# Kernel tuning notes

Measured on AMD Instinct MI355X. Metric: run time of the kernel, lower is better.

Reference implementation:

```python
import jax, jax.numpy as jnp
import numpy as np

E = 16          # num_experts
H = 2048        # hidden_size
I = 768         # moe_intermediate_size
T = 2048        # tokens (batch*seq)
K = 2           # top_k


def setup_inputs() -> dict:
    key = jax.random.key(0)
    k1, k2, k3, k4, k5 = jax.random.split(key, 5)
    hidden_states = jax.random.normal(k1, (T, H), dtype=jnp.float32)
    top_k_index = jax.random.randint(k2, (T, K), 0, E, dtype=jnp.int32)
    w = jax.random.uniform(k3, (T, K), dtype=jnp.float32)
    top_k_weights = w / jnp.sum(w, axis=-1, keepdims=True)  # softmax-like router weights
    init_std = 0.02
    gate_up_proj = jax.random.normal(k4, (E, 2 * I, H), dtype=jnp.float32) * init_std
    down_proj = jax.random.normal(k5, (E, H, I), dtype=jnp.float32) * init_std
    return {
        "hidden_states": hidden_states,
        "top_k_index": top_k_index,
        "top_k_weights": top_k_weights,
        "gate_up_proj": gate_up_proj,
        "down_proj": down_proj,
    }


def reference(hidden_states, top_k_index, top_k_weights, gate_up_proj, down_proj):
    # Combine matrix C[t, e] = sum_k top_k_weights[t, k] * 1[top_k_index[t,k] == e]
    # Tokens not routed to expert e get weight 0, so the dense-masked compute
    # below is mathematically identical to the per-expert gather/scatter loop.
    t_idx = jnp.arange(T)[:, None]
    C = jnp.zeros((T, E), dtype=hidden_states.dtype).at[t_idx, top_k_index].add(top_k_weights)

    # gate/up projection for every (token, expert): [T, E, 2I]
    gu = jnp.einsum('th,egh->teg', hidden_states, gate_up_proj)
    gate, up = jnp.split(gu, 2, axis=-1)                  # [T, E, I] each
    mid = jax.nn.silu(gate) * up                          # SwiGLU, [T, E, I]
    # down projection fused with routed combine weights -> [T, H]
    out = jnp.einsum('tei,ehi,te->th', mid, down_proj, C)
    return out
```

## Files before the change

kernel.cpp:

```cpp
#include <hip/hip_runtime.h>

#define TTOK  2048
#define HID   2048
#define IMID  768
#define NEXP  16
#define NPAIR 4096
#define NSLOT 4224
#define BM    128
#define BK    64
#define MAXT  48
#define LDB   72
#define ABUF  (128 * 64)

typedef __attribute__((ext_vector_type(8))) short  short8;
typedef __attribute__((ext_vector_type(4))) float  floatx4;
typedef __attribute__((ext_vector_type(2))) unsigned uint2v;

__device__ __forceinline__ unsigned pk2(float a, float b) {
    union { float f; unsigned u; } x{a}, y{b};
    unsigned ra = (x.u + 0x7FFFu + ((x.u >> 16) & 1u)) >> 16;
    unsigned rb = (y.u + 0x7FFFu + ((y.u >> 16) & 1u)) & 0xFFFF0000u;
    return ra | rb;
}

__device__ __forceinline__ short f2bf(float f) {
    union { float f; unsigned u; } v; v.f = f;
    return (short)((v.u + 0x7FFFu + ((v.u >> 16) & 1u)) >> 16);
}

__device__ __forceinline__ short8 cvt8(float4 a, float4 b) {
    union { unsigned u[4]; short8 s; } r;
    r.u[0] = pk2(a.x, a.y); r.u[1] = pk2(a.z, a.w);
    r.u[2] = pk2(b.x, b.y); r.u[3] = pk2(b.z, b.w);
    return r.s;
}

__device__ __forceinline__ void async_cp16(const void* g, void* l) {
    __builtin_amdgcn_global_load_lds(
        (const __attribute__((address_space(1))) void*)g,
        (__attribute__((address_space(3))) void*)l, 16, 0, 0);
}

__global__ __launch_bounds__(256) void k_pre(
    const float* __restrict__ hs, const int* __restrict__ idx,
    const float* __restrict__ tkw, int* __restrict__ ntiles,
    int4* __restrict__ tiles, int* __restrict__ tok,
    float* __restrict__ wgt, short* __restrict__ X)
{
    const int tid = threadIdx.x;
    if (blockIdx.x == 0) {
        __shared__ int cnt[NEXP], cur[NEXP];
        if (tid < NEXP) cnt[tid] = 0;
        __syncthreads();
        for (int i = tid; i < NPAIR; i += 256) atomicAdd(&cnt[idx[i]], 1);
        __syncthreads();
        if (tid == 0) {
            int s = 0, nt = 0;
            for (int e = 0; e < NEXP; e++) {
                cur[e] = s;
                int n = cnt[e];
                for (int tt = 0; tt * BM < n; tt++) {
                    tiles[nt] = make_int4(e, s + tt * BM, min(BM, n - tt * BM), 0);
                    nt++;
                }
                s += n;
            }
            *ntiles = nt;
        }
        __syncthreads();
        for (int i = tid; i < NPAIR; i += 256) {
            int e = idx[i];
            int p = atomicAdd(&cur[e], 1);
            tok[p] = i >> 1;
            wgt[p] = tkw[i];
        }
        for (int i = NPAIR + tid; i < NSLOT; i += 256) { tok[i] = 0; wgt[i] = 0.0f; }
    } else {
        const int row = blockIdx.x - 1;
        const float* src = hs + (size_t)row * HID + tid * 8;
        float4 a = *(const float4*)src;
        float4 b = *(const float4*)(src + 4);
        *(short8*)(X + (size_t)row * HID + tid * 8) = cvt8(a, b);
    }
}

__global__ __launch_bounds__(256, 2) void k_gemm1(
    const float* __restrict__ gup, const short* __restrict__ X,
    const int* __restrict__ ntiles, const int4* __restrict__ tiles,
    const int* __restrict__ tok, const float* __restrict__ wgt,
    short* __restrict__ mid)
{
    if ((int)blockIdx.y >= *ntiles) return;
    const int4 td = tiles[blockIdx.y];
    const int e = td.x, rowstart = td.y, nvalid = td.z;
    const int ct = blockIdx.x;

    __shared__ short sA[2 * ABUF];
    __shared__ short sB[128 * LDB];
    __shared__ int   s_tok[BM];
    __shared__ float s_w[BM];

    const int tid = threadIdx.x;
    if (tid < BM) { s_tok[tid] = tok[rowstart + tid]; s_w[tid] = wgt[rowstart + tid]; }
    __syncthreads();

    const int wave = tid >> 6, lane = tid & 63;
    const int m16 = lane & 15, quad = lane >> 4;

    const int lrow = tid >> 3;
    const int gsw  = (tid & 7) ^ (lrow & 7);
    const short* aga[4];
#pragma unroll
    for (int j = 0; j < 4; j++)
        aga[j] = X + (size_t)s_tok[lrow + j * 32] * HID + gsw * 8;

    const int colgrp = tid & 15;
    const int rowoff = tid >> 4;
    const float* bgate = gup + ((size_t)e * (2 * IMID) + ct * 64) * HID;
    const float* bup   = bgate + (size_t)IMID * HID;

    float4 br[8];
    auto loadB = [&](int k0) {
#pragma unroll
        for (int i = 0; i < 8; i++) {
            int brow = i * 16 + rowoff;
            const float* p = (i < 4) ? (bgate + (size_t)brow * HID)
                                     : (bup + (size_t)(brow - 64) * HID);
            br[i] = *(const float4*)(p + k0 + colgrp * 4);
        }
    };
    auto issueA = [&](int k0, short* dst) {
#pragma unroll
        for (int j = 0; j < 4; j++)
            async_cp16(aga[j] + k0, dst + j * 2048 + wave * 512);
    };

    const int Wm = (wave >> 1) << 6;
    const int Wi = (wave & 1) << 5;
    floatx4 ag[4][2], au[4][2];
#pragma unroll
    for (int a = 0; a < 4; a++)
#pragma unroll
        for (int b = 0; b < 2; b++) { ag[a][b] = (floatx4)0.0f; au[a][b] = (floatx4)0.0f; }

    loadB(0);
    issueA(0, sA);

    const int nsteps = HID / BK;
    for (int ks = 0; ks < nsteps; ks++) {
        short* Acur  = sA + (ks & 1) * ABUF;
        short* Anext = sA + ((ks + 1) & 1) * ABUF;

#pragma unroll
        for (int i = 0; i < 8; i++) {
            int brow = i * 16 + rowoff;
            uint2v w2;
            w2.x = pk2(br[i].x, br[i].y);
            w2.y = pk2(br[i].z, br[i].w);
            *(uint2v*)&sB[brow * LDB + colgrp * 4] = w2;
        }
        __syncthreads();

        if (ks + 1 < nsteps) {
            issueA((ks + 1) * BK, Anext);
            loadB((ks + 1) * BK);
        }

#pragma unroll
        for (int h = 0; h < 2; h++) {
            short8 af[4];
#pragma unroll
            for (int mf = 0; mf < 4; mf++) {
                int row = Wm + mf * 16 + m16;
                int gc = (h * 4 + quad) ^ (row & 7);
                af[mf] = *(const short8*)&Acur[row * 64 + gc * 8];
            }
#pragma unroll
            for (int nf = 0; nf < 2; nf++) {
                const short8 bg = *(const short8*)&sB[(Wi + nf * 16 + m16) * LDB + h * 32 + quad * 8];
                const short8 bu = *(const short8*)&sB[(64 + Wi + nf * 16 + m16) * LDB + h * 32 + quad * 8];
#pragma unroll
                for (int mf = 0; mf < 4; mf++) {
                    ag[mf][nf] = __builtin_amdgcn_mfma_f32_16x16x32_bf16(af[mf], bg, ag[mf][nf], 0, 0, 0);
                    au[mf][nf] = __builtin_amdgcn_mfma_f32_16x16x32_bf16(af[mf], bu, au[mf][nf], 0, 0, 0);
                }
            }
        }
        __syncthreads();
    }

#pragma unroll
    for (int mf = 0; mf < 4; mf++) {
#pragma unroll
        for (int r = 0; r < 4; r++) {
            int m = Wm + mf * 16 + quad * 4 + r;
            if (m < nvalid) {
                float w = s_w[m];
                size_t rowp = (size_t)(rowstart + m) * IMID + ct * 64;
#pragma unroll
                for (int nf = 0; nf < 2; nf++) {
                    float g = ag[mf][nf][r], u = au[mf][nf][r];
                    float val = g / (1.0f + __expf(-g)) * u * w;
                    mid[rowp + Wi + nf * 16 + m16] = f2bf(val);
                }
            }
        }
    }
}

__global__ __launch_bounds__(256, 2) void k_gemm2(
    const float* __restrict__ down, const short* __restrict__ mid,
    const int* __restrict__ ntiles, const int4* __restrict__ tiles,
    const int* __restrict__ tok, float* __restrict__ out)
{
    if ((int)blockIdx.y >= *ntiles) return;
    const int4 td = tiles[blockIdx.y];
    const int e = td.x, rowstart = td.y, nvalid = td.z;
    const int ct = blockIdx.x;

    __shared__ short sA[2 * ABUF];
    __shared__ short sB[128 * LDB];
    __shared__ int   s_tok[BM];

    const int tid = threadIdx.x;
    if (tid < BM) s_tok[tid] = tok[rowstart + tid];
    __syncthreads();

    const int wave = tid >> 6, lane = tid & 63;
    const int m16 = lane & 15, quad = lane >> 4;

    const int lrow = tid >> 3;
    const int gsw  = (tid & 7) ^ (lrow & 7);
    const short* aga[4];
#pragma unroll
    for (int j = 0; j < 4; j++)
        aga[j] = mid + (size_t)(rowstart + lrow + j * 32) * IMID + gsw * 8;

    const int colgrp = tid & 15;
    const int rowoff = tid >> 4;
    const float* bbase = down + ((size_t)e * HID + ct * 128) * IMID;

    float4 br[8];
    auto loadB = [&](int k0) {
#pragma unroll
        for (int i = 0; i < 8; i++)
            br[i] = *(const float4*)(bbase + (size_t)(i * 16 + rowoff) * IMID + k0 + colgrp * 4);
    };
    auto issueA = [&](int k0, short* dst) {
#pragma unroll
        for (int j = 0; j < 4; j++)
            async_cp16(aga[j] + k0, dst + j * 2048 + wave * 512);
    };

    const int Wm = (wave >> 1) << 6;
    const int Wn = (wave & 1) << 6;
    floatx4 acc[4][4];
#pragma unroll
    for (int a = 0; a < 4; a++)
#pragma unroll
        for (int b = 0; b < 4; b++) acc[a][b] = (floatx4)0.0f;

    loadB(0);
    issueA(0, sA);

    const int nsteps = IMID / BK;
    for (int ks = 0; ks < nsteps; ks++) {
        short* Acur  = sA + (ks & 1) * ABUF;
        short* Anext = sA + ((ks + 1) & 1) * ABUF;

#pragma unroll
        for (int i = 0; i < 8; i++) {
            int brow = i * 16 + rowoff;
            uint2v w2;
            w2.x = pk2(br[i].x, br[i].y);
            w2.y = pk2(br[i].z, br[i].w);
            *(uint2v*)&sB[brow * LDB + colgrp * 4] = w2;
        }
        __syncthreads();

        if (ks + 1 < nsteps) {
            issueA((ks + 1) * BK, Anext);
            loadB((ks + 1) * BK);
        }

#pragma unroll
        for (int h = 0; h < 2; h++) {
            short8 af[4];
#pragma unroll
            for (int mf = 0; mf < 4; mf++) {
                int row = Wm + mf * 16 + m16;
                int gc = (h * 4 + quad) ^ (row & 7);
                af[mf] = *(const short8*)&Acur[row * 64 + gc * 8];
            }
#pragma unroll
            for (int nf = 0; nf < 4; nf++) {
                const short8 bf_ = *(const short8*)&sB[(Wn + nf * 16 + m16) * LDB + h * 32 + quad * 8];
#pragma unroll
                for (int mf = 0; mf < 4; mf++)
                    acc[mf][nf] = __builtin_amdgcn_mfma_f32_16x16x32_bf16(af[mf], bf_, acc[mf][nf], 0, 0, 0);
            }
        }
        __syncthreads();
    }

#pragma unroll
    for (int mf = 0; mf < 4; mf++) {
#pragma unroll
        for (int r = 0; r < 4; r++) {
            int m = Wm + mf * 16 + quad * 4 + r;
            if (m < nvalid) {
                int t = s_tok[m];
                float* op = out + (size_t)t * HID + ct * 128;
#pragma unroll
                for (int nf = 0; nf < 4; nf++)
                    atomicAdd(op + Wn + nf * 16 + m16, acc[mf][nf][r]);
            }
        }
    }
}

extern "C" void kernel_launch(void* const* d_in, const int* in_sizes, int n_in,
                              void* d_out, int out_size, void* d_ws, size_t ws_size,
                              hipStream_t stream) {
    const float* hs   = (const float*)d_in[0];
    const int*   idx  = (const int*)d_in[1];
    const float* tkw  = (const float*)d_in[2];
    const float* gup  = (const float*)d_in[3];
    const float* down = (const float*)d_in[4];
    float* out = (float*)d_out;

    char* ws = (char*)d_ws;
    int*   ntiles = (int*)ws;
    int4*  tiles  = (int4*)(ws + 16);
    int*   tok    = (int*)(ws + 1024);
    float* wgt    = (float*)(ws + 1024 + NSLOT * 4);
    short* mid    = (short*)(ws + 36864);
    short* X      = (short*)(ws + 36864 + (size_t)NSLOT * IMID * 2);

    hipMemsetAsync(d_out, 0, (size_t)TTOK * HID * sizeof(float), stream);
    k_pre  <<<2049, 256, 0, stream>>>(hs, idx, tkw, ntiles, tiles, tok, wgt, X);
    k_gemm1<<<dim3(IMID / 64, MAXT), 256, 0, stream>>>(gup, X, ntiles, tiles, tok, wgt, mid);
    k_gemm2<<<dim3(HID / 128, MAXT), 256, 0, stream>>>(down, mid, ntiles, tiles, tok, out);
}
```

Before: 435.9 us.

## Pre-convert expert weights to bf16 and stage both GEMM operands via async LDS copies

Adds a conversion pass to the preprocessing kernel that writes bf16 copies of the gate_up and down weight tensors into the workspace. Both GEMM kernels then stream the B operand from those bf16 buffers with direct global-to-LDS async copies, using the same XOR swizzle as the A operand. B is now double-buffered in LDS, which removes the per-step register load, pack and LDS store of fp32 weights and one barrier per step. The cost is an extra full read of the fp32 weights plus a bf16 write on every call, a larger workspace footprint, and twice the LDS for B.

```diff
diff --git a/kernel.cpp b/kernel.cpp
--- a/kernel.cpp
+++ b/kernel.cpp
@@ -9,12 +9,13 @@
 #define BM    128
 #define BK    64
 #define MAXT  48
-#define LDB   72
 #define ABUF  (128 * 64)
+
+#define GUP_CHUNKS 24576
+#define DN_CHUNKS  12288
 
 typedef __attribute__((ext_vector_type(8))) short  short8;
 typedef __attribute__((ext_vector_type(4))) float  floatx4;
-typedef __attribute__((ext_vector_type(2))) unsigned uint2v;
 
 __device__ __forceinline__ unsigned pk2(float a, float b) {
     union { float f; unsigned u; } x{a}, y{b};
@@ -43,12 +44,15 @@
 
 __global__ __launch_bounds__(256) void k_pre(
     const float* __restrict__ hs, const int* __restrict__ idx,
-    const float* __restrict__ tkw, int* __restrict__ ntiles,
+    const float* __restrict__ tkw, const float* __restrict__ gup,
+    const float* __restrict__ down, int* __restrict__ ntiles,
     int4* __restrict__ tiles, int* __restrict__ tok,
-    float* __restrict__ wgt, short* __restrict__ X)
+    float* __restrict__ wgt, short* __restrict__ X,
+    short* __restrict__ gupb, short* __restrict__ downb)
 {
     const int tid = threadIdx.x;
-    if (blockIdx.x == 0) {
+    const int bx  = (int)blockIdx.x;
+    if (bx == 0) {
         __shared__ int cnt[NEXP], cur[NEXP];
         if (tid < NEXP) cnt[tid] = 0;
         __syncthreads();
@@ -75,17 +79,29 @@
             wgt[p] = tkw[i];
         }
         for (int i = NPAIR + tid; i < NSLOT; i += 256) { tok[i] = 0; wgt[i] = 0.0f; }
-    } else {
-        const int row = blockIdx.x - 1;
+    } else if (bx <= TTOK) {
+        const int row = bx - 1;
         const float* src = hs + (size_t)row * HID + tid * 8;
         float4 a = *(const float4*)src;
         float4 b = *(const float4*)(src + 4);
         *(short8*)(X + (size_t)row * HID + tid * 8) = cvt8(a, b);
+    } else if (bx <= TTOK + GUP_CHUNKS) {
+        const size_t c = (size_t)(bx - 1 - TTOK);
+        const float* src = gup + c * 2048 + tid * 8;
+        float4 a = *(const float4*)src;
+        float4 b = *(const float4*)(src + 4);
+        *(short8*)(gupb + c * 2048 + tid * 8) = cvt8(a, b);
+    } else {
+        const size_t c = (size_t)(bx - 1 - TTOK - GUP_CHUNKS);
+        const float* src = down + c * 2048 + tid * 8;
+        float4 a = *(const float4*)src;
+        float4 b = *(const float4*)(src + 4);
+        *(short8*)(downb + c * 2048 + tid * 8) = cvt8(a, b);
     }
 }
 
 __global__ __launch_bounds__(256, 2) void k_gemm1(
-    const float* __restrict__ gup, const short* __restrict__ X,
+    const short* __restrict__ gupb, const short* __restrict__ X,
     const int* __restrict__ ntiles, const int4* __restrict__ tiles,
     const int* __restrict__ tok, const float* __restrict__ wgt,
     short* __restrict__ mid)
@@ -96,7 +112,7 @@
     const int ct = blockIdx.x;
 
     __shared__ short sA[2 * ABUF];
-    __shared__ short sB[128 * LDB];
+    __shared__ short sB[2 * ABUF];
     __shared__ int   s_tok[BM];
     __shared__ float s_w[BM];
 
@@ -110,29 +126,24 @@
     const int lrow = tid >> 3;
     const int gsw  = (tid & 7) ^ (lrow & 7);
     const short* aga[4];
+    const short* bga[4];
 #pragma unroll
     for (int j = 0; j < 4; j++)
         aga[j] = X + (size_t)s_tok[lrow + j * 32] * HID + gsw * 8;
-
-    const int colgrp = tid & 15;
-    const int rowoff = tid >> 4;
-    const float* bgate = gup + ((size_t)e * (2 * IMID) + ct * 64) * HID;
-    const float* bup   = bgate + (size_t)IMID * HID;
-
-    float4 br[8];
-    auto loadB = [&](int k0) {
-#pragma unroll
-        for (int i = 0; i < 8; i++) {
-            int brow = i * 16 + rowoff;
-            const float* p = (i < 4) ? (bgate + (size_t)brow * HID)
-                                     : (bup + (size_t)(brow - 64) * HID);
-            br[i] = *(const float4*)(p + k0 + colgrp * 4);
-        }
-    };
-    auto issueA = [&](int k0, short* dst) {
+    const short* gb = gupb + (size_t)e * (2 * IMID) * HID + gsw * 8;
+#pragma unroll
+    for (int j = 0; j < 2; j++) {
+        bga[j]     = gb + (size_t)(ct * 64 + lrow + j * 32) * HID;
+        bga[j + 2] = gb + (size_t)(IMID + ct * 64 + lrow + j * 32) * HID;
+    }
+
+    auto stage = [&](int k0, short* dA, short* dB) {
 #pragma unroll
         for (int j = 0; j < 4; j++)
-            async_cp16(aga[j] + k0, dst + j * 2048 + wave * 512);
+            async_cp16(aga[j] + k0, dA + j * 2048 + wave * 512);
+#pragma unroll
+        for (int j = 0; j < 4; j++)
+            async_cp16(bga[j] + k0, dB + j * 2048 + wave * 512);
     };
 
     const int Wm = (wave >> 1) << 6;
@@ -143,28 +154,15 @@
 #pragma unroll
         for (int b = 0; b < 2; b++) { ag[a][b] = (floatx4)0.0f; au[a][b] = (floatx4)0.0f; }
 
-    loadB(0);
-    issueA(0, sA);
+    stage(0, sA, sB);
+    __syncthreads();
 
     const int nsteps = HID / BK;
     for (int ks = 0; ks < nsteps; ks++) {
-        short* Acur  = sA + (ks & 1) * ABUF;
-        short* Anext = sA + ((ks + 1) & 1) * ABUF;
-
-#pragma unroll
-        for (int i = 0; i < 8; i++) {
-            int brow = i * 16 + rowoff;
-            uint2v w2;
-            w2.x = pk2(br[i].x, br[i].y);
-            w2.y = pk2(br[i].z, br[i].w);
-            *(uint2v*)&sB[brow * LDB + colgrp * 4] = w2;
-        }
-        __syncthreads();
-
-        if (ks + 1 < nsteps) {
-            issueA((ks + 1) * BK, Anext);
-            loadB((ks + 1) * BK);
-        }
+        const short* Acur = sA + (ks & 1) * ABUF;
+        const short* Bcur = sB + (ks & 1) * ABUF;
+        if (ks + 1 < nsteps)
+            stage((ks + 1) * BK, sA + ((ks + 1) & 1) * ABUF, sB + ((ks + 1) & 1) * ABUF);
 
 #pragma unroll
         for (int h = 0; h < 2; h++) {
@@ -177,8 +175,10 @@
             }
 #pragma unroll
             for (int nf = 0; nf < 2; nf++) {
-                const short8 bg = *(const short8*)&sB[(Wi + nf * 16 + m16) * LDB + h * 32 + quad * 8];
-                const short8 bu = *(const short8*)&sB[(64 + Wi + nf * 16 + m16) * LDB + h * 32 + quad * 8];
+                int brow = Wi + nf * 16 + m16;
+                int gcb = (h * 4 + quad) ^ (brow & 7);
+                const short8 bg = *(const short8*)&Bcur[brow * 64 + gcb * 8];
+                const short8 bu = *(const short8*)&Bcur[(64 + brow) * 64 + gcb * 8];
 #pragma unroll
                 for (int mf = 0; mf < 4; mf++) {
                     ag[mf][nf] = __builtin_amdgcn_mfma_f32_16x16x32_bf16(af[mf], bg, ag[mf][nf], 0, 0, 0);
@@ -209,7 +209,7 @@
 }
 
 __global__ __launch_bounds__(256, 2) void k_gemm2(
-    const float* __restrict__ down, const short* __restrict__ mid,
+    const short* __restrict__ downb, const short* __restrict__ mid,
     const int* __restrict__ ntiles, const int4* __restrict__ tiles,
     const int* __restrict__ tok, float* __restrict__ out)
 {
@@ -219,7 +219,7 @@
     const int ct = blockIdx.x;
 
     __shared__ short sA[2 * ABUF];
-    __shared__ short sB[128 * LDB];
+    __shared__ short sB[2 * ABUF];
     __shared__ int   s_tok[BM];
 
     const int tid = threadIdx.x;
@@ -232,24 +232,22 @@
     const int lrow = tid >> 3;
     const int gsw  = (tid & 7) ^ (lrow & 7);
     const short* aga[4];
+    const short* bga[4];
 #pragma unroll
     for (int j = 0; j < 4; j++)
         aga[j] = mid + (size_t)(rowstart + lrow + j * 32) * IMID + gsw * 8;
-
-    const int colgrp = tid & 15;
-    const int rowoff = tid >> 4;
-    const float* bbase = down + ((size_t)e * HID + ct * 128) * IMID;
-
-    float4 br[8];
-    auto loadB = [&](int k0) {
-#pragma unroll
-        for (int i = 0; i < 8; i++)
-            br[i] = *(const float4*)(bbase + (size_t)(i * 16 + rowoff) * IMID + k0 + colgrp * 4);
-    };
-    auto issueA = [&](int k0, short* dst) {
+    const short* db = downb + ((size_t)e * HID + ct * 128) * IMID + gsw * 8;
+#pragma unroll
+    for (int j = 0; j < 4; j++)
+        bga[j] = db + (size_t)(lrow + j * 32) * IMID;
+
+    auto stage = [&](int k0, short* dA, short* dB) {
 #pragma unroll
         for (int j = 0; j < 4; j++)
-            async_cp16(aga[j] + k0, dst + j * 2048 + wave * 512);
+            async_cp16(aga[j] + k0, dA + j * 2048 + wave * 512);
+#pragma unroll
+        for (int j = 0; j < 4; j++)
+            async_cp16(bga[j] + k0, dB + j * 2048 + wave * 512);
     };
 
     const int Wm = (wave >> 1) << 6;
@@ -260,28 +258,15 @@
 #pragma unroll
         for (int b = 0; b < 4; b++) acc[a][b] = (floatx4)0.0f;
 
-    loadB(0);
-    issueA(0, sA);
+    stage(0, sA, sB);
+    __syncthreads();
 
     const int nsteps = IMID / BK;
     for (int ks = 0; ks < nsteps; ks++) {
-        short* Acur  = sA + (ks & 1) * ABUF;
-        short* Anext = sA + ((ks + 1) & 1) * ABUF;
-
-#pragma unroll
-        for (int i = 0; i < 8; i++) {
-            int brow = i * 16 + rowoff;
-            uint2v w2;
-            w2.x = pk2(br[i].x, br[i].y);
-            w2.y = pk2(br[i].z, br[i].w);
-            *(uint2v*)&sB[brow * LDB + colgrp * 4] = w2;
-        }
-        __syncthreads();
-
-        if (ks + 1 < nsteps) {
-            issueA((ks + 1) * BK, Anext);
-            loadB((ks + 1) * BK);
-        }
+        const short* Acur = sA + (ks & 1) * ABUF;
+        const short* Bcur = sB + (ks & 1) * ABUF;
+        if (ks + 1 < nsteps)
+            stage((ks + 1) * BK, sA + ((ks + 1) & 1) * ABUF, sB + ((ks + 1) & 1) * ABUF);
 
 #pragma unroll
         for (int h = 0; h < 2; h++) {
@@ -294,7 +279,9 @@
             }
 #pragma unroll
             for (int nf = 0; nf < 4; nf++) {
-                const short8 bf_ = *(const short8*)&sB[(Wn + nf * 16 + m16) * LDB + h * 32 + quad * 8];
+                int brow = Wn + nf * 16 + m16;
+                int gcb = (h * 4 + quad) ^ (brow & 7);
+                const short8 bf_ = *(const short8*)&Bcur[brow * 64 + gcb * 8];
 #pragma unroll
                 for (int mf = 0; mf < 4; mf++)
                     acc[mf][nf] = __builtin_amdgcn_mfma_f32_16x16x32_bf16(af[mf], bf_, acc[mf][nf], 0, 0, 0);
@@ -336,9 +323,12 @@
     float* wgt    = (float*)(ws + 1024 + NSLOT * 4);
     short* mid    = (short*)(ws + 36864);
     short* X      = (short*)(ws + 36864 + (size_t)NSLOT * IMID * 2);
+    short* gupb   = (short*)(ws + (16u << 20));
+    short* downb  = (short*)(ws + (16u << 20) + (size_t)NEXP * 2 * IMID * HID * 2);
 
     hipMemsetAsync(d_out, 0, (size_t)TTOK * HID * sizeof(float), stream);
-    k_pre  <<<2049, 256, 0, stream>>>(hs, idx, tkw, ntiles, tiles, tok, wgt, X);
-    k_gemm1<<<dim3(IMID / 64, MAXT), 256, 0, stream>>>(gup, X, ntiles, tiles, tok, wgt, mid);
-    k_gemm2<<<dim3(HID / 128, MAXT), 256, 0, stream>>>(down, mid, ntiles, tiles, tok, out);
-}
+    k_pre  <<<1 + TTOK + GUP_CHUNKS + DN_CHUNKS, 256, 0, stream>>>(
+        hs, idx, tkw, gup, down, ntiles, tiles, tok, wgt, X, gupb, downb);
+    k_gemm1<<<dim3(IMID / 64, MAXT), 256, 0, stream>>>(gupb, X, ntiles, tiles, tok, wgt, mid);
+    k_gemm2<<<dim3(HID / 128, MAXT), 256, 0, stream>>>(downb, mid, ntiles, tiles, tok, out);
+}
```

After: 484.0 us. 11.0% more time.
